# Kernel tuning notes

Hardware: AMD Instinct MI355X
Metric: run time of the kernel (lower is better)

The kernel has to match this reference:

```python
import jax, jax.numpy as jnp
import numpy as np

B, I, O, K = 4096, 1024, 1024, 16

def setup_inputs() -> dict:
    key = jax.random.key(0)
    k1, k2 = jax.random.split(key)
    x = jax.random.normal(k1, (B, I), dtype=jnp.float32)
    weights = jax.random.normal(k2, (O, I, K), dtype=jnp.float32)
    bias = jnp.zeros((O,), dtype=jnp.float32)
    centers = jnp.linspace(-1.0, 1.0, K, dtype=jnp.float32)
    widths = jnp.full((K,), 0.1, dtype=jnp.float32)
    return {"x": x, "weights": weights, "bias": bias, "centers": centers, "widths": widths}

def reference(x, weights, bias, centers, widths):
    # Gaussian RBF basis: [B, I, K]
    diff = x[:, :, None] - centers[None, None, :]
    kernels = jnp.exp(-(diff ** 2) / (2.0 * widths[None, None, :] ** 2))
    # Contraction over input_dim and num_kernels (GEMM-equivalent)
    out = jnp.einsum('bik,oik->bo', kernels, weights)
    return out + bias
```

## Files before the change

kernel.cpp:

```cpp
#include <hip/hip_runtime.h>
#include <hip/hip_bf16.h>


#define B_DIM 4096
#define I_DIM 1024
#define O_DIM 1024
#define NK 16
#define KD (I_DIM * NK)

typedef unsigned short u16;
typedef __attribute__((ext_vector_type(8))) __bf16 bf16x8;
typedef __attribute__((ext_vector_type(4))) float f32x4;
typedef __attribute__((ext_vector_type(8))) unsigned short u16x8;

typedef const __attribute__((address_space(1))) unsigned short gu16;
typedef __attribute__((address_space(3))) unsigned short lu16;

static __device__ __forceinline__ u16 f2bf(float f) {
  unsigned u = __float_as_uint(f);
  u += 0x7FFFu + ((u >> 16) & 1u);
  return (u16)(u >> 16);
}

__global__ void __launch_bounds__(256) rbf_feat(const float* __restrict__ x,
                                                u16* __restrict__ feat,
                                                const float* __restrict__ centers,
                                                const float* __restrict__ widths) {
  const int idx = blockIdx.x * 256 + threadIdx.x;
  const float xv = x[idx];
  u16x8 lo, hi;
#pragma unroll
  for (int k = 0; k < 16; ++k) {
    const float c = centers[k];
    const float w = widths[k];
    const float s = -0.5f * __builtin_amdgcn_rcpf(w * w);
    const float d = xv - c;
    const u16 h = f2bf(__expf(d * d * s));
    if (k < 8) lo[k] = h; else hi[k - 8] = h;
  }
  u16x8* dst = (u16x8*)(feat + (size_t)idx * 16);
  dst[0] = lo;
  dst[1] = hi;
}

__global__ void __launch_bounds__(256) cvt_w(const float4* __restrict__ w,
                                             u16x8* __restrict__ wb) {
  const size_t i = (size_t)blockIdx.x * 256 + threadIdx.x;
  const float4 a = w[2 * i];
  const float4 b = w[2 * i + 1];
  u16x8 o;
  o[0] = f2bf(a.x); o[1] = f2bf(a.y); o[2] = f2bf(a.z); o[3] = f2bf(a.w);
  o[4] = f2bf(b.x); o[5] = f2bf(b.y); o[6] = f2bf(b.z); o[7] = f2bf(b.w);
  wb[i] = o;
}

static __device__ __forceinline__ void stage_half(const u16* __restrict__ g,
                                                  u16* __restrict__ lds, int t) {
#pragma unroll
  for (int j = 0; j < 2; ++j) {
    const int chunk = j * 512 + t;
    const int row = chunk >> 3, slot = chunk & 7;
    const int c = slot ^ (row & 7);
    __builtin_amdgcn_global_load_lds((gu16*)(g + (size_t)row * KD + c * 8),
                                     (lu16*)(lds + chunk * 8), 16, 0, 0);
  }
}

#define NT 64

__global__ void __launch_bounds__(512, 2)
gemm8(const u16* __restrict__ A, const u16* __restrict__ Bm,
      float* __restrict__ part) {
  __shared__ u16 sA[2][2][128 * 64];
  __shared__ u16 sB[2][2][128 * 64];

  const int t = threadIdx.x;
  const int lin = blockIdx.x + 16 * (blockIdx.y + 4 * blockIdx.z);
  const int work = (lin & 7) * 32 + (lin >> 3);
  const int bm = work & 15;
  const int bn = (work >> 4) & 3;
  const int kz = work >> 6;
  const int wid = t >> 6, l = t & 63;
  const int wr = wid >> 2, wc = wid & 3;
  const int lm = l & 15, lk = l >> 4;

  const u16* aT = A + (size_t)(bm * 256) * KD + kz * 4096;
  const u16* bT = Bm + (size_t)(bn * 256) * KD + kz * 4096;

  const int swz0 = ((0 * 4 + lk) ^ (lm & 7)) * 8;
  const int swz1 = ((1 * 4 + lk) ^ (lm & 7)) * 8;
  const int arow = wr * 64 + lm;
  const int brow = wc * 32 + lm;

  f32x4 acc[8][4];
#pragma unroll
  for (int i = 0; i < 8; ++i)
#pragma unroll
    for (int j = 0; j < 4; ++j)
      acc[i][j] = (f32x4){0.f, 0.f, 0.f, 0.f};

  stage_half(aT, &sA[0][0][0], t);
  stage_half(aT + (size_t)128 * KD, &sA[0][1][0], t);
  stage_half(bT, &sB[0][0][0], t);
  stage_half(bT + (size_t)128 * KD, &sB[0][1][0], t);
  stage_half(bT + 64, &sB[1][0][0], t);
  stage_half(aT + 64, &sA[1][0][0], t);
  asm volatile("s_waitcnt vmcnt(4)" ::: "memory");
  __builtin_amdgcn_s_barrier();

  for (int T = 0; T < NT; ++T) {
    const int c = T & 1;

    bf16x8 aq[4][2], b0[2][2], b1[2][2];
#pragma unroll
    for (int mi = 0; mi < 4; ++mi) {
      aq[mi][0] = *(const bf16x8*)&sA[c][0][(arow + mi * 16) * 64 + swz0];
      aq[mi][1] = *(const bf16x8*)&sA[c][0][(arow + mi * 16) * 64 + swz1];
    }
#pragma unroll
    for (int ni = 0; ni < 2; ++ni) {
      b0[ni][0] = *(const bf16x8*)&sB[c][0][(brow + ni * 16) * 64 + swz0];
      b0[ni][1] = *(const bf16x8*)&sB[c][0][(brow + ni * 16) * 64 + swz1];
      b1[ni][0] = *(const bf16x8*)&sB[c][1][(brow + ni * 16) * 64 + swz0];
      b1[ni][1] = *(const bf16x8*)&sB[c][1][(brow + ni * 16) * 64 + swz1];
    }
    if (T + 1 < NT) {
      stage_half(aT + (size_t)128 * KD + (T + 1) * 64, &sA[(T + 1) & 1][1][0], t);
      stage_half(bT + (size_t)128 * KD + (T + 1) * 64, &sB[(T + 1) & 1][1][0], t);
    }

    __builtin_amdgcn_s_setprio(1);
#pragma unroll
    for (int mi = 0; mi < 4; ++mi)
#pragma unroll
      for (int ni = 0; ni < 2; ++ni)
#pragma unroll
        for (int kk = 0; kk < 2; ++kk)
          acc[mi][ni] = __builtin_amdgcn_mfma_f32_16x16x32_bf16(
              aq[mi][kk], b0[ni][kk], acc[mi][ni], 0, 0, 0);
#pragma unroll
    for (int mi = 0; mi < 4; ++mi)
#pragma unroll
      for (int ni = 0; ni < 2; ++ni)
#pragma unroll
        for (int kk = 0; kk < 2; ++kk)
          acc[mi][2 + ni] = __builtin_amdgcn_mfma_f32_16x16x32_bf16(
              aq[mi][kk], b1[ni][kk], acc[mi][2 + ni], 0, 0, 0);
    __builtin_amdgcn_s_setprio(0);

    asm volatile("s_waitcnt lgkmcnt(0)" ::: "memory");
    __builtin_amdgcn_sched_barrier(0);
    __builtin_amdgcn_s_barrier();

    bf16x8 aq2[4][2];
#pragma unroll
    for (int mi = 0; mi < 4; ++mi) {
      aq2[mi][0] = *(const bf16x8*)&sA[c][1][(arow + mi * 16) * 64 + swz0];
      aq2[mi][1] = *(const bf16x8*)&sA[c][1][(arow + mi * 16) * 64 + swz1];
    }
    if (T + 2 < NT) {
      stage_half(bT + (T + 2) * 64, &sB[T & 1][0][0], t);
      stage_half(aT + (T + 2) * 64, &sA[T & 1][0][0], t);
    }

    __builtin_amdgcn_s_setprio(1);
#pragma unroll
    for (int mi = 0; mi < 4; ++mi)
#pragma unroll
      for (int ni = 0; ni < 2; ++ni)
#pragma unroll
        for (int kk = 0; kk < 2; ++kk)
          acc[4 + mi][2 + ni] = __builtin_amdgcn_mfma_f32_16x16x32_bf16(
              aq2[mi][kk], b1[ni][kk], acc[4 + mi][2 + ni], 0, 0, 0);
#pragma unroll
    for (int mi = 0; mi < 4; ++mi)
#pragma unroll
      for (int ni = 0; ni < 2; ++ni)
#pragma unroll
        for (int kk = 0; kk < 2; ++kk)
          acc[4 + mi][ni] = __builtin_amdgcn_mfma_f32_16x16x32_bf16(
              aq2[mi][kk], b0[ni][kk], acc[4 + mi][ni], 0, 0, 0);
    __builtin_amdgcn_s_setprio(0);

    if (T + 2 < NT) asm volatile("s_waitcnt vmcnt(4)" ::: "memory");
    else            asm volatile("s_waitcnt vmcnt(0)" ::: "memory");
    __builtin_amdgcn_s_barrier();
  }

  float* pW = part + (size_t)kz * ((size_t)B_DIM * O_DIM);
#pragma unroll
  for (int qa = 0; qa < 2; ++qa)
#pragma unroll
    for (int mi = 0; mi < 4; ++mi)
#pragma unroll
      for (int qb = 0; qb < 2; ++qb)
#pragma unroll
        for (int ni = 0; ni < 2; ++ni) {
          const int row0 = bm * 256 + qa * 128 + wr * 64 + mi * 16 + lk * 4;
          const int col = bn * 256 + qb * 128 + wc * 32 + ni * 16 + lm;
#pragma unroll
          for (int j = 0; j < 4; ++j)
            pW[(size_t)(row0 + j) * O_DIM + col] = acc[qa * 4 + mi][qb * 2 + ni][j];
        }
}

__global__ void __launch_bounds__(256) reduce4(const float4* __restrict__ p,
                                               const float4* __restrict__ bias4,
                                               float4* __restrict__ out) {
  const int i = blockIdx.x * 256 + threadIdx.x;
  const size_t s = (size_t)B_DIM * O_DIM / 4;
  const float4 a = p[i], b = p[i + s], c = p[i + 2 * s], d = p[i + 3 * s];
  const float4 bb = bias4[i & 255];
  float4 r;
  r.x = a.x + b.x + c.x + d.x + bb.x;
  r.y = a.y + b.y + c.y + d.y + bb.y;
  r.z = a.z + b.z + c.z + d.z + bb.z;
  r.w = a.w + b.w + c.w + d.w + bb.w;
  out[i] = r;
}

#define BM 128
#define BN 64
#define BK 64

__global__ void __launch_bounds__(256, 2) gemm_bt(const u16* __restrict__ A,
                                                  const u16* __restrict__ Bm,
                                                  const float* __restrict__ bias,
                                                  float* __restrict__ C) {
  __shared__ u16 sA[BM * BK];
  __shared__ u16 sB[BN * BK];

  const int t = threadIdx.x;
  const int bm = blockIdx.x, bn = blockIdx.y;
  const int wid = t >> 6, l = t & 63;
  const int wr = wid >> 1, wc = wid & 1;
  const int lm = l & 15, lk = l >> 4;

  const u16* aG = A + (size_t)bm * BM * KD;
  const u16* bG = Bm + (size_t)bn * BN * KD;

  f32x4 acc[4][2];
#pragma unroll
  for (int mi = 0; mi < 4; ++mi)
#pragma unroll
    for (int ni = 0; ni < 2; ++ni)
      acc[mi][ni] = (f32x4){0.f, 0.f, 0.f, 0.f};

  for (int kt = 0; kt < KD; kt += BK) {
#pragma unroll
    for (int j = 0; j < 4; ++j) {
      const int chunk = j * 256 + t;
      const int row = chunk >> 3, slot = chunk & 7;
      const int c = slot ^ (row & 7);
      __builtin_amdgcn_global_load_lds((gu16*)(aG + (size_t)row * KD + kt + c * 8),
                                       (lu16*)(sA + chunk * 8), 16, 0, 0);
    }
#pragma unroll
    for (int j = 0; j < 2; ++j) {
      const int chunk = j * 256 + t;
      const int row = chunk >> 3, slot = chunk & 7;
      const int c = slot ^ (row & 7);
      __builtin_amdgcn_global_load_lds((gu16*)(bG + (size_t)row * KD + kt + c * 8),
                                       (lu16*)(sB + chunk * 8), 16, 0, 0);
    }
    __syncthreads();
#pragma unroll
    for (int kk = 0; kk < 2; ++kk) {
      const int s = (kk * 4 + lk) ^ (lm & 7);
      bf16x8 af[4], bfr[2];
#pragma unroll
      for (int mi = 0; mi < 4; ++mi)
        af[mi] = *(const bf16x8*)(sA + (wr * 64 + mi * 16 + lm) * BK + s * 8);
#pragma unroll
      for (int ni = 0; ni < 2; ++ni)
        bfr[ni] = *(const bf16x8*)(sB + (wc * 32 + ni * 16 + lm) * BK + s * 8);
#pragma unroll
      for (int mi = 0; mi < 4; ++mi)
#pragma unroll
        for (int ni = 0; ni < 2; ++ni)
          acc[mi][ni] = __builtin_amdgcn_mfma_f32_16x16x32_bf16(af[mi], bfr[ni],
                                                                acc[mi][ni], 0, 0, 0);
    }
    __syncthreads();
  }

#pragma unroll
  for (int ni = 0; ni < 2; ++ni) {
    const int col = bn * BN + wc * 32 + ni * 16 + lm;
    const float bv = bias[col];
#pragma unroll
    for (int mi = 0; mi < 4; ++mi) {
      const int row0 = bm * BM + wr * 64 + mi * 16 + lk * 4;
#pragma unroll
      for (int j = 0; j < 4; ++j)
        C[(size_t)(row0 + j) * O_DIM + col] = acc[mi][ni][j] + bv;
    }
  }
}

extern "C" void kernel_launch(void* const* d_in, const int* in_sizes, int n_in,
                              void* d_out, int out_size, void* d_ws, size_t ws_size,
                              hipStream_t stream) {
  const float* x = (const float*)d_in[0];
  const float* w = (const float*)d_in[1];
  const float* bias = (const float*)d_in[2];
  const float* centers = (const float*)d_in[3];
  const float* widths = (const float*)d_in[4];
  float* out = (float*)d_out;

  u16* feat = (u16*)d_ws;
  u16* wb = (u16*)((char*)d_ws + (size_t)B_DIM * KD * 2);
  float* part = (float*)((char*)d_ws + (size_t)B_DIM * KD * 2 + (size_t)O_DIM * KD * 2);

  rbf_feat<<<(B_DIM * I_DIM) / 256, 256, 0, stream>>>(x, feat, centers, widths);
  cvt_w<<<(O_DIM * KD) / (256 * 8), 256, 0, stream>>>((const float4*)w, (u16x8*)wb);

  const size_t need = (size_t)B_DIM * KD * 2 + (size_t)O_DIM * KD * 2 +
                      4ull * B_DIM * O_DIM * 4;
  if (ws_size >= need) {
    dim3 grid(B_DIM / 256, O_DIM / 256, 4);
    gemm8<<<grid, 512, 0, stream>>>(feat, wb, part);
    reduce4<<<(B_DIM * O_DIM / 4) / 256, 256, 0, stream>>>(
        (const float4*)part, (const float4*)bias, (float4*)out);
  } else {
    dim3 grid(B_DIM / BM, O_DIM / BN);
    gemm_bt<<<grid, 256, 0, stream>>>(feat, wb, bias, out);
  }
}
```

Measured before the change: 185.6 us.

## Fuse prep kernels and replace split-K partial buffer with atomic adds

New measurement: 196.7 us. 1.06x slower.

```diff
diff --git a/kernel.cpp b/kernel.cpp
--- a/kernel.cpp
+++ b/kernel.cpp
@@ -22,36 +22,48 @@
   return (u16)(u >> 16);
 }
 
-__global__ void __launch_bounds__(256) rbf_feat(const float* __restrict__ x,
-                                                u16* __restrict__ feat,
-                                                const float* __restrict__ centers,
-                                                const float* __restrict__ widths) {
-  const int idx = blockIdx.x * 256 + threadIdx.x;
-  const float xv = x[idx];
-  u16x8 lo, hi;
-#pragma unroll
-  for (int k = 0; k < 16; ++k) {
-    const float c = centers[k];
-    const float w = widths[k];
-    const float s = -0.5f * __builtin_amdgcn_rcpf(w * w);
-    const float d = xv - c;
-    const u16 h = f2bf(__expf(d * d * s));
-    if (k < 8) lo[k] = h; else hi[k - 8] = h;
-  }
-  u16x8* dst = (u16x8*)(feat + (size_t)idx * 16);
-  dst[0] = lo;
-  dst[1] = hi;
-}
-
-__global__ void __launch_bounds__(256) cvt_w(const float4* __restrict__ w,
-                                             u16x8* __restrict__ wb) {
-  const size_t i = (size_t)blockIdx.x * 256 + threadIdx.x;
-  const float4 a = w[2 * i];
-  const float4 b = w[2 * i + 1];
-  u16x8 o;
-  o[0] = f2bf(a.x); o[1] = f2bf(a.y); o[2] = f2bf(a.z); o[3] = f2bf(a.w);
-  o[4] = f2bf(b.x); o[5] = f2bf(b.y); o[6] = f2bf(b.z); o[7] = f2bf(b.w);
-  wb[i] = o;
+#define PREP_RBF_BLOCKS (B_DIM * I_DIM / 256)
+#define PREP_CVT_BLOCKS (O_DIM * KD / (256 * 8))
+#define PREP_INIT_BLOCKS (B_DIM * O_DIM / 4 / 256)
+
+__global__ void __launch_bounds__(256) prep(const float* __restrict__ x,
+                                            u16* __restrict__ feat,
+                                            const float4* __restrict__ w,
+                                            u16x8* __restrict__ wb,
+                                            const float* __restrict__ centers,
+                                            const float* __restrict__ widths,
+                                            const float4* __restrict__ bias4,
+                                            float4* __restrict__ out4) {
+  const int blk = blockIdx.x;
+  const int t = threadIdx.x;
+  if (blk < PREP_RBF_BLOCKS) {
+    const int idx = blk * 256 + t;
+    const float xv = x[idx];
+    u16x8 lo, hi;
+#pragma unroll
+    for (int k = 0; k < 16; ++k) {
+      const float c = centers[k];
+      const float wd = widths[k];
+      const float s = -0.5f * __builtin_amdgcn_rcpf(wd * wd);
+      const float d = xv - c;
+      const u16 h = f2bf(__expf(d * d * s));
+      if (k < 8) lo[k] = h; else hi[k - 8] = h;
+    }
+    u16x8* dst = (u16x8*)(feat + (size_t)idx * 16);
+    dst[0] = lo;
+    dst[1] = hi;
+  } else if (blk < PREP_RBF_BLOCKS + PREP_CVT_BLOCKS) {
+    const size_t i = (size_t)(blk - PREP_RBF_BLOCKS) * 256 + t;
+    const float4 a = w[2 * i];
+    const float4 b = w[2 * i + 1];
+    u16x8 o;
+    o[0] = f2bf(a.x); o[1] = f2bf(a.y); o[2] = f2bf(a.z); o[3] = f2bf(a.w);
+    o[4] = f2bf(b.x); o[5] = f2bf(b.y); o[6] = f2bf(b.z); o[7] = f2bf(b.w);
+    wb[i] = o;
+  } else {
+    const int i = (blk - PREP_RBF_BLOCKS - PREP_CVT_BLOCKS) * 256 + t;
+    out4[i] = bias4[i & 255];
+  }
 }
 
 static __device__ __forceinline__ void stage_half(const u16* __restrict__ g,
@@ -70,7 +82,7 @@
 
 __global__ void __launch_bounds__(512, 2)
 gemm8(const u16* __restrict__ A, const u16* __restrict__ Bm,
-      float* __restrict__ part) {
+      float* __restrict__ out) {
   __shared__ u16 sA[2][2][128 * 64];
   __shared__ u16 sB[2][2][128 * 64];
 
@@ -187,7 +199,6 @@
     __builtin_amdgcn_s_barrier();
   }
 
-  float* pW = part + (size_t)kz * ((size_t)B_DIM * O_DIM);
 #pragma unroll
   for (int qa = 0; qa < 2; ++qa)
 #pragma unroll
@@ -200,28 +211,46 @@
           const int col = bn * 256 + qb * 128 + wc * 32 + ni * 16 + lm;
 #pragma unroll
           for (int j = 0; j < 4; ++j)
-            pW[(size_t)(row0 + j) * O_DIM + col] = acc[qa * 4 + mi][qb * 2 + ni][j];
+            unsafeAtomicAdd(&out[(size_t)(row0 + j) * O_DIM + col],
+                            acc[qa * 4 + mi][qb * 2 + ni][j]);
         }
-}
-
-__global__ void __launch_bounds__(256) reduce4(const float4* __restrict__ p,
-                                               const float4* __restrict__ bias4,
-                                               float4* __restrict__ out) {
-  const int i = blockIdx.x * 256 + threadIdx.x;
-  const size_t s = (size_t)B_DIM * O_DIM / 4;
-  const float4 a = p[i], b = p[i + s], c = p[i + 2 * s], d = p[i + 3 * s];
-  const float4 bb = bias4[i & 255];
-  float4 r;
-  r.x = a.x + b.x + c.x + d.x + bb.x;
-  r.y = a.y + b.y + c.y + d.y + bb.y;
-  r.z = a.z + b.z + c.z + d.z + bb.z;
-  r.w = a.w + b.w + c.w + d.w + bb.w;
-  out[i] = r;
 }
 
 #define BM 128
 #define BN 64
 #define BK 64
+
+__global__ void __launch_bounds__(256) rbf_feat_fb(const float* __restrict__ x,
+                                                   u16* __restrict__ feat,
+                                                   const float* __restrict__ centers,
+                                                   const float* __restrict__ widths) {
+  const int idx = blockIdx.x * 256 + threadIdx.x;
+  const float xv = x[idx];
+  u16x8 lo, hi;
+#pragma unroll
+  for (int k = 0; k < 16; ++k) {
+    const float c = centers[k];
+    const float w = widths[k];
+    const float s = -0.5f * __builtin_amdgcn_rcpf(w * w);
+    const float d = xv - c;
+    const u16 h = f2bf(__expf(d * d * s));
+    if (k < 8) lo[k] = h; else hi[k - 8] = h;
+  }
+  u16x8* dst = (u16x8*)(feat + (size_t)idx * 16);
+  dst[0] = lo;
+  dst[1] = hi;
+}
+
+__global__ void __launch_bounds__(256) cvt_w_fb(const float4* __restrict__ w,
+                                                u16x8* __restrict__ wb) {
+  const size_t i = (size_t)blockIdx.x * 256 + threadIdx.x;
+  const float4 a = w[2 * i];
+  const float4 b = w[2 * i + 1];
+  u16x8 o;
+  o[0] = f2bf(a.x); o[1] = f2bf(a.y); o[2] = f2bf(a.z); o[3] = f2bf(a.w);
+  o[4] = f2bf(b.x); o[5] = f2bf(b.y); o[6] = f2bf(b.z); o[7] = f2bf(b.w);
+  wb[i] = o;
+}
 
 __global__ void __launch_bounds__(256, 2) gemm_bt(const u16* __restrict__ A,
                                                   const u16* __restrict__ Bm,
@@ -310,19 +339,17 @@
 
   u16* feat = (u16*)d_ws;
   u16* wb = (u16*)((char*)d_ws + (size_t)B_DIM * KD * 2);
-  float* part = (float*)((char*)d_ws + (size_t)B_DIM * KD * 2 + (size_t)O_DIM * KD * 2);
-
-  rbf_feat<<<(B_DIM * I_DIM) / 256, 256, 0, stream>>>(x, feat, centers, widths);
-  cvt_w<<<(O_DIM * KD) / (256 * 8), 256, 0, stream>>>((const float4*)w, (u16x8*)wb);
-
-  const size_t need = (size_t)B_DIM * KD * 2 + (size_t)O_DIM * KD * 2 +
-                      4ull * B_DIM * O_DIM * 4;
+  const size_t need = (size_t)B_DIM * KD * 2 + (size_t)O_DIM * KD * 2;
+
   if (ws_size >= need) {
+    prep<<<PREP_RBF_BLOCKS + PREP_CVT_BLOCKS + PREP_INIT_BLOCKS, 256, 0, stream>>>(
+        x, feat, (const float4*)w, (u16x8*)wb, centers, widths,
+        (const float4*)bias, (float4*)out);
     dim3 grid(B_DIM / 256, O_DIM / 256, 4);
-    gemm8<<<grid, 512, 0, stream>>>(feat, wb, part);
-    reduce4<<<(B_DIM * O_DIM / 4) / 256, 256, 0, stream>>>(
-        (const float4*)part, (const float4*)bias, (float4*)out);
+    gemm8<<<grid, 512, 0, stream>>>(feat, wb, out);
   } else {
+    rbf_feat_fb<<<(B_DIM * I_DIM) / 256, 256, 0, stream>>>(x, feat, centers, widths);
+    cvt_w_fb<<<(O_DIM * KD) / (256 * 8), 256, 0, stream>>>((const float4*)w, (u16x8*)wb);
     dim3 grid(B_DIM / BM, O_DIM / BN);
     gemm_bt<<<grid, 256, 0, stream>>>(feat, wb, bias, out);
   }
```
